# Optimization experiments

Hardware: AMD Instinct MI355X
Metric: run time of the kernel (lower is better)

## Reference

```python
import jax, jax.numpy as jnp
import numpy as np

STATE_DIM = 256
ACT_LEN = 16
LATENT = 256
ENC = 512
SLOPE = 0.01  # torch.nn.LeakyReLU() default


def _leaky(x):
    return jnp.where(x >= 0, x, SLOPE * x)


def setup_inputs() -> dict:
    key = jax.random.key(0)
    ks = jax.random.split(key, 16)
    B, T = 64, 1024
    D = STATE_DIM + 2 * ACT_LEN
    s = lambda k, shp, fan_in: jax.random.normal(k, shp, dtype=jnp.float32) * (1.0 / np.sqrt(fan_in))
    return {
        "padded_input": jax.random.normal(ks[0], (B, T, D), dtype=jnp.float32),
        # encoder: Linear(state,enc)+leaky, Linear(enc,enc)+leaky, Linear(enc,latent)+leaky
        "enc_w1": s(ks[1], (STATE_DIM, ENC), STATE_DIM), "enc_b1": jnp.zeros((ENC,), jnp.float32),
        "enc_w2": s(ks[2], (ENC, ENC), ENC),             "enc_b2": jnp.zeros((ENC,), jnp.float32),
        "enc_w3": s(ks[3], (ENC, LATENT), ENC),          "enc_b3": jnp.zeros((LATENT,), jnp.float32),
        # latent dynamics (bias-free)
        "A_w": s(ks[4], (LATENT, LATENT), LATENT),
        "B_w": s(ks[5], (ACT_LEN, LATENT), ACT_LEN),
        # decoder: Linear(latent,enc)+leaky, Linear(enc,enc)+leaky, Linear(enc,state)
        "dec_w1": s(ks[6], (LATENT, ENC), LATENT),       "dec_b1": jnp.zeros((ENC,), jnp.float32),
        "dec_w2": s(ks[7], (ENC, ENC), ENC),             "dec_b2": jnp.zeros((ENC,), jnp.float32),
        "dec_w3": s(ks[8], (ENC, STATE_DIM), ENC),       "dec_b3": jnp.zeros((STATE_DIM,), jnp.float32),
    }


def reference(padded_input, enc_w1, enc_b1, enc_w2, enc_b2, enc_w3, enc_b3,
              A_w, B_w, dec_w1, dec_b1, dec_w2, dec_b2, dec_w3, dec_b3):
    # slice features: [state | u_t | u_t1]
    x_t = padded_input[:, :, :STATE_DIM]                       # [B,T,S]
    u_t1 = padded_input[:, :, STATE_DIM + ACT_LEN:]            # [B,T,A]

    # encoder MLP
    h = _leaky(x_t @ enc_w1 + enc_b1)
    h = _leaky(h @ enc_w2 + enc_b2)
    z_t = _leaky(h @ enc_w3 + enc_b3)                          # [B,T,L]

    # reset_probability=0, nwarmup=0: t=0 uses z_t[:,0], then pure recurrence
    # z1[t] = A z1[t-1] + B u_t1[t]
    Bu = u_t1 @ B_w                                            # [B,T,L]

    def step(prev, bu_t):
        new = prev @ A_w + bu_t                                # [B,L]
        return new, new

    _, z1 = jax.lax.scan(step, z_t[:, 0, :], jnp.swapaxes(Bu, 0, 1))
    z_t1 = jnp.swapaxes(z1, 0, 1)                              # [B,T,L]

    # decoder MLP (last layer linear)
    h = _leaky(z_t1 @ dec_w1 + dec_b1)
    h = _leaky(h @ dec_w2 + dec_b2)
    x_t1 = h @ dec_w3 + dec_b3                                 # [B,T,S]
    return x_t1
```

## Files before the change

kernel.cpp:

```cpp
#include <hip/hip_runtime.h>

constexpr int Bb  = 64;
constexpr int Tt  = 1024;
constexpr int Dd  = 288;
constexpr int Ss  = 256;
constexpr int ALa = 16;
constexpr int Ll  = 256;
constexpr int Ee  = 512;
constexpr int CC  = 8;
constexpr int NCh = 128;
constexpr int NSC = 16;
constexpr int SC  = 8;
constexpr int DEC_CHUNKS = 8;
constexpr int DEC_ROWS = (Bb*Tt)/DEC_CHUNKS;

#define LKY(v) ((v) >= 0.f ? (v) : 0.01f*(v))

using f32x4  = __attribute__((ext_vector_type(4))) float;
using short8 = __attribute__((ext_vector_type(8))) short;
typedef unsigned short ushort_t;

__device__ __forceinline__ unsigned short f2bf(float f){
  unsigned int u = __float_as_uint(f);
  u = (u + 0x7fffu + ((u >> 16) & 1u)) >> 16;
  return (unsigned short)u;
}
__device__ __forceinline__ float bf2f(unsigned short h){
  return __uint_as_float(((unsigned int)h) << 16);
}

__global__ __launch_bounds__(256) void enc_dense(
    const float* __restrict__ xin, int xstride,
    const float* __restrict__ W, const float* __restrict__ bias,
    float* __restrict__ out, int K, int N, int act)
{
  int b = blockIdx.x, col0 = blockIdx.y * 32;
  int tid = threadIdx.x;
  int tx = tid & 31, tk = tid >> 5;
  __shared__ float x[512];
  __shared__ float part[8][33];
  for (int k = tid; k < K; k += 256) x[k] = xin[(long)b*xstride + k];
  __syncthreads();
  int j = col0 + tx;
  float p0=0.f,p1=0.f,p2=0.f,p3=0.f;
  int iters = K >> 3;
  #pragma unroll 2
  for (int i = 0; i < iters; i += 4){
    int k0 = tk + 8*i;
    p0 = fmaf(x[k0     ], W[(long)(k0     )*N + j], p0);
    p1 = fmaf(x[k0 +  8], W[(long)(k0 +  8)*N + j], p1);
    p2 = fmaf(x[k0 + 16], W[(long)(k0 + 16)*N + j], p2);
    p3 = fmaf(x[k0 + 24], W[(long)(k0 + 24)*N + j], p3);
  }
  part[tk][tx] = (p0+p1)+(p2+p3);
  __syncthreads();
  if (tid < 32){
    float s = part[0][tid];
    #pragma unroll
    for (int q = 1; q < 8; ++q) s += part[q][tid];
    s += bias[col0 + tid];
    out[b*N + col0 + tid] = act ? LKY(s) : s;
  }
}

__global__ __launch_bounds__(256) void matmul_g(
    const float* __restrict__ X, const float* __restrict__ Y,
    float* __restrict__ Cf, ushort_t* __restrict__ Ch, ushort_t* __restrict__ Cl)
{
  int i = blockIdx.x;
  int tid = threadIdx.x;
  int jg = tid & 63, tk = tid >> 6;
  __shared__ float row[256];
  __shared__ float4 part[4][64];
  if (tid < 256) row[tid] = X[i*256 + tid];
  __syncthreads();
  int j4 = jg*4;
  float4 p0 = make_float4(0,0,0,0), p1 = make_float4(0,0,0,0);
  int kb = tk*64;
  #pragma unroll 4
  for (int k = kb; k < kb+64; k += 2){
    float x0 = row[k], x1 = row[k+1];
    float4 y0 = *(const float4*)&Y[(k  )*256 + j4];
    float4 y1 = *(const float4*)&Y[(k+1)*256 + j4];
    p0.x = fmaf(x0,y0.x,p0.x); p0.y = fmaf(x0,y0.y,p0.y);
    p0.z = fmaf(x0,y0.z,p0.z); p0.w = fmaf(x0,y0.w,p0.w);
    p1.x = fmaf(x1,y1.x,p1.x); p1.y = fmaf(x1,y1.y,p1.y);
    p1.z = fmaf(x1,y1.z,p1.z); p1.w = fmaf(x1,y1.w,p1.w);
  }
  p0.x+=p1.x; p0.y+=p1.y; p0.z+=p1.z; p0.w+=p1.w;
  part[tk][jg] = p0;
  __syncthreads();
  if (tid < 64){
    float4 s = part[0][tid];
    #pragma unroll
    for (int q = 1; q < 4; ++q){
      float4 v = part[q][tid];
      s.x+=v.x; s.y+=v.y; s.z+=v.z; s.w+=v.w;
    }
    int j = tid*4;
    if (Cf) *(float4*)&Cf[i*256 + j] = s;
    if (Ch){
      float vv[4] = {s.x,s.y,s.z,s.w};
      #pragma unroll
      for (int e = 0; e < 4; ++e){
        ushort_t h = f2bf(vv[e]);
        int o = ((i>>3)*256 + j + e)*8 + (i&7);
        Ch[o] = h; Cl[o] = f2bf(vv[e] - bf2f(h));
      }
    }
  }
}

__global__ __launch_bounds__(256) void prep_w(
    const float* __restrict__ W, ushort_t* __restrict__ Wh,
    ushort_t* __restrict__ Wl, int N)
{
  int o = blockIdx.x*256 + threadIdx.x;
  int j = o & 7;
  int rest = o >> 3;
  int n = rest % N;
  int t8 = rest / N;
  int k = t8*8 + j;
  float v = W[k*N + n];
  ushort_t h = f2bf(v);
  Wh[o] = h;
  Wl[o] = f2bf(v - bf2f(h));
}

__global__ __launch_bounds__(256) void prep_bw(
    const float* __restrict__ B, ushort_t* __restrict__ Bh, ushort_t* __restrict__ Bl)
{
  int o = blockIdx.x*256 + threadIdx.x;
  int j = o & 7, rest = o >> 3;
  int n = rest & 255, kq = rest >> 8;
  int k = kq*8 + j;
  float v = (k < ALa) ? B[k*256 + n] : 0.f;
  ushort_t h = f2bf(v);
  Bh[o] = h; Bl[o] = f2bf(v - bf2f(h));
}

__device__ __forceinline__ void load_afrag(
    const ushort_t* __restrict__ P, int kq, int m0, short8* dst)
{
  #pragma unroll
  for (int mt = 0; mt < 4; ++mt)
    dst[mt] = *(const short8*)&P[((long)kq*256 + m0 + mt*16)*8];
}

__global__ __launch_bounds__(256) void scan_mfma(
    const float* __restrict__ in0,
    const ushort_t* __restrict__ AtH, const ushort_t* __restrict__ AtL,
    const ushort_t* __restrict__ BtH, const ushort_t* __restrict__ BtL,
    float* __restrict__ wend, float* __restrict__ zout)
{
  int chunk = blockIdx.x;
  int tid = threadIdx.x;
  int wave = tid >> 6, lane = tid & 63;
  int quad = lane >> 4, l16 = lane & 15;
  int mwave = wave * 64;
  int m0 = mwave + l16;

  __shared__ ushort_t StH[16384];
  __shared__ ushort_t StL[16384];

  short8 Bfh[4], Bfl[4];
  #pragma unroll
  for (int mt = 0; mt < 4; ++mt){
    int off = ((quad)*256 + m0 + mt*16)*8;
    Bfh[mt] = *(const short8*)&BtH[off];
    Bfl[mt] = *(const short8*)&BtL[off];
  }

  f32x4 acc[4][4];
  #pragma unroll
  for (int mt = 0; mt < 4; ++mt)
    #pragma unroll
    for (int nt = 0; nt < 4; ++nt) acc[mt][nt] = (f32x4){0.f,0.f,0.f,0.f};

  const float* ubase[4];
  #pragma unroll
  for (int nt = 0; nt < 4; ++nt)
    ubase[nt] = in0 + (long)(nt*16 + l16)*(Tt*Dd) + (Ss + ALa) + quad*8;

  short8 Ahb[2][4], Alb[2][4];

  for (int tt = 0; tt < CC; ++tt){
    int t = chunk*CC + tt;
    float4 uq[4][2];
    #pragma unroll
    for (int nt = 0; nt < 4; ++nt){
      if (quad < 2){
        const float* up = ubase[nt] + (long)t*Dd;
        uq[nt][0] = *(const float4*)up;
        uq[nt][1] = *(const float4*)(up + 4);
      } else {
        uq[nt][0] = make_float4(0,0,0,0); uq[nt][1] = make_float4(0,0,0,0);
      }
    }

    if (tt > 0){
      load_afrag(AtH, 0*4 + quad, m0, Ahb[0]);
      load_afrag(AtL, 0*4 + quad, m0, Alb[0]);
      #pragma unroll
      for (int kt = 0; kt < 8; ++kt){
        int cur = kt & 1;
        if (kt < 7){
          load_afrag(AtH, (kt+1)*4 + quad, m0, Ahb[cur^1]);
          load_afrag(AtL, (kt+1)*4 + quad, m0, Alb[cur^1]);
        }
        short8 Sbh[4], Sbl[4];
        #pragma unroll
        for (int nt = 0; nt < 4; ++nt){
          int off = ((kt*4 + quad)*64 + nt*16 + l16)*8;
          Sbh[nt] = *(const short8*)&StH[off];
          Sbl[nt] = *(const short8*)&StL[off];
        }
        #pragma unroll
        for (int mt = 0; mt < 4; ++mt)
          #pragma unroll
          for (int nt = 0; nt < 4; ++nt){
            acc[mt][nt] = __builtin_amdgcn_mfma_f32_16x16x32_bf16(Ahb[cur][mt], Sbh[nt], acc[mt][nt], 0,0,0);
            acc[mt][nt] = __builtin_amdgcn_mfma_f32_16x16x32_bf16(Ahb[cur][mt], Sbl[nt], acc[mt][nt], 0,0,0);
            acc[mt][nt] = __builtin_amdgcn_mfma_f32_16x16x32_bf16(Alb[cur][mt], Sbh[nt], acc[mt][nt], 0,0,0);
          }
      }
    }

    short8 uh[4], ul[4];
    #pragma unroll
    for (int nt = 0; nt < 4; ++nt){
      float v[8] = {uq[nt][0].x,uq[nt][0].y,uq[nt][0].z,uq[nt][0].w,
                    uq[nt][1].x,uq[nt][1].y,uq[nt][1].z,uq[nt][1].w};
      ushort_t hs[8], ls[8];
      #pragma unroll
      for (int j = 0; j < 8; ++j){
        hs[j] = f2bf(v[j]);
        ls[j] = f2bf(v[j] - bf2f(hs[j]));
      }
      uh[nt] = *(const short8*)hs; ul[nt] = *(const short8*)ls;
    }
    #pragma unroll
    for (int mt = 0; mt < 4; ++mt)
      #pragma unroll
      for (int nt = 0; nt < 4; ++nt){
        acc[mt][nt] = __builtin_amdgcn_mfma_f32_16x16x32_bf16(Bfh[mt], uh[nt], acc[mt][nt], 0,0,0);
        acc[mt][nt] = __builtin_amdgcn_mfma_f32_16x16x32_bf16(Bfh[mt], ul[nt], acc[mt][nt], 0,0,0);
        acc[mt][nt] = __builtin_amdgcn_mfma_f32_16x16x32_bf16(Bfl[mt], uh[nt], acc[mt][nt], 0,0,0);
      }

    __syncthreads();

    #pragma unroll
    for (int mt = 0; mt < 4; ++mt){
      int mb = mwave + mt*16 + quad*4;
      #pragma unroll
      for (int nt = 0; nt < 4; ++nt){
        int n = nt*16 + l16;
        f32x4 v = acc[mt][nt];
        *(float4*)&zout[((long)n*Tt + t)*Ll + mb] = make_float4(v[0],v[1],v[2],v[3]);
        if (tt == CC-1)
          *(float4*)&wend[((long)chunk*Bb + n)*Ll + mb] = make_float4(v[0],v[1],v[2],v[3]);
        #pragma unroll
        for (int reg = 0; reg < 4; ++reg){
          int m = mb + reg;
          ushort_t h = f2bf(v[reg]);
          ushort_t l = f2bf(v[reg] - bf2f(h));
          int so = ((m>>3)*64 + n)*8 + (m&7);
          StH[so] = h; StL[so] = l;
        }
        acc[mt][nt] = (f32x4){0.f,0.f,0.f,0.f};
      }
    }
    __syncthreads();
  }
}

__device__ __forceinline__ void frag_init_state512(
    const float* __restrict__ src, ushort_t* StH, ushort_t* StL, int tid)
{
  #pragma unroll
  for (int it = 0; it < 4; ++it){
    int idx = tid + it*512;
    int m8 = idx >> 6, n = idx & 63;
    const float* p = src + (long)n*256 + m8*8;
    float4 v0 = *(const float4*)p;
    float4 v1 = *(const float4*)(p + 4);
    float vv[8] = {v0.x,v0.y,v0.z,v0.w,v1.x,v1.y,v1.z,v1.w};
    ushort_t hs[8], ls[8];
    #pragma unroll
    for (int j = 0; j < 8; ++j){
      hs[j] = f2bf(vv[j]);
      ls[j] = f2bf(vv[j] - bf2f(hs[j]));
    }
    *(uint4*)&StH[(m8*64 + n)*8] = *(const uint4*)hs;
    *(uint4*)&StL[(m8*64 + n)*8] = *(const uint4*)ls;
  }
}

__device__ __forceinline__ void p2_load_A(
    const ushort_t* __restrict__ PH, const ushort_t* __restrict__ PL,
    int wave, int lane, short8 Ah[2][8], short8 Al[2][8])
{
  int quad = lane >> 4, l16 = lane & 15;
  int m0 = wave*32 + l16;
  #pragma unroll
  for (int kt = 0; kt < 8; ++kt){
    int kq = kt*4 + quad;
    #pragma unroll
    for (int mt = 0; mt < 2; ++mt){
      Ah[mt][kt] = *(const short8*)&PH[((long)kq*256 + m0 + mt*16)*8];
      Al[mt][kt] = *(const short8*)&PL[((long)kq*256 + m0 + mt*16)*8];
    }
  }
}

__device__ __forceinline__ void ks_gemm_body(
    const ushort_t* __restrict__ PH, const ushort_t* __restrict__ PL,
    const float* __restrict__ accsrc, const float* __restrict__ bsrc,
    float* __restrict__ outp, ushort_t* StH, ushort_t* StL)
{
  int tid = threadIdx.x;
  int wave = tid >> 6, lane = tid & 63;
  int quad = lane >> 4, l16 = lane & 15;
  int mwave = wave*32;

  short8 Ah[2][8], Al[2][8];
  p2_load_A(PH, PL, wave, lane, Ah, Al);
  frag_init_state512(bsrc, StH, StL, tid);

  f32x4 acc[2][4];
  #pragma unroll
  for (int mt = 0; mt < 2; ++mt){
    int mb = mwave + mt*16 + quad*4;
    #pragma unroll
    for (int nt = 0; nt < 4; ++nt){
      int n = nt*16 + l16;
      float4 v = *(const float4*)&accsrc[(long)n*256 + mb];
      acc[mt][nt] = (f32x4){v.x, v.y, v.z, v.w};
    }
  }
  __syncthreads();

  #pragma unroll
  for (int kt = 0; kt < 8; ++kt){
    #pragma unroll
    for (int nt = 0; nt < 4; ++nt){
      int off = ((kt*4 + quad)*64 + nt*16 + l16)*8;
      short8 Sbh = *(const short8*)&StH[off];
      short8 Sbl = *(const short8*)&StL[off];
      #pragma unroll
      for (int mt = 0; mt < 2; ++mt){
        acc[mt][nt] = __builtin_amdgcn_mfma_f32_16x16x32_bf16(Ah[mt][kt], Sbh, acc[mt][nt], 0,0,0);
        acc[mt][nt] = __builtin_amdgcn_mfma_f32_16x16x32_bf16(Ah[mt][kt], Sbl, acc[mt][nt], 0,0,0);
        acc[mt][nt] = __builtin_amdgcn_mfma_f32_16x16x32_bf16(Al[mt][kt], Sbh, acc[mt][nt], 0,0,0);
      }
    }
  }

  #pragma unroll
  for (int mt = 0; mt < 2; ++mt){
    int mb = mwave + mt*16 + quad*4;
    #pragma unroll
    for (int nt = 0; nt < 4; ++nt){
      int n = nt*16 + l16;
      f32x4 v = acc[mt][nt];
      *(float4*)&outp[(long)n*256 + mb] = make_float4(v[0],v[1],v[2],v[3]);
    }
  }
}

__device__ __forceinline__ const float* ks_src(
    const float* __restrict__ in, const float* __restrict__ z0,
    const float* __restrict__ pbend, int c, int init_mode)
{
  if (!init_mode) return in + (long)c*(Bb*Ll);
  return (c == 0) ? z0 : (pbend + (long)(8*c - 1)*(Bb*Ll));
}

__global__ __launch_bounds__(512) void ks_round(
    const ushort_t* __restrict__ PH, const ushort_t* __restrict__ PL,
    const float* __restrict__ in, const float* __restrict__ z0,
    const float* __restrict__ pbend,
    float* __restrict__ out, long outStride, int d, int local_seg, int init_mode)
{
  int c = blockIdx.x;
  int tid = threadIdx.x;
  int pos = local_seg ? (c & 7) : c;
  const float* src_c = ks_src(in, z0, pbend, c, init_mode);
  float* op = out + (long)c*outStride;

  if (pos < d){
    const float4* s4p = (const float4*)src_c;
    float4* d4p = (float4*)op;
    #pragma unroll
    for (int it = 0; it < 8; ++it) d4p[tid + it*512] = s4p[tid + it*512];
    return;
  }
  const float* src_cd = ks_src(in, z0, pbend, c - d, init_mode);
  __shared__ ushort_t StH[16384], StL[16384];
  ks_gemm_body(PH, PL, src_c, src_cd, op, StH, StL);
}

__global__ __launch_bounds__(512) void replay_corr(
    const ushort_t* __restrict__ A8PH, const ushort_t* __restrict__ A8PL,
    const float* __restrict__ pb, float* __restrict__ inits)
{
  int i = blockIdx.x + 1;
  int s = blockIdx.y;
  __shared__ ushort_t StH[16384], StL[16384];
  ks_gemm_body(A8PH + (long)(i-1)*65536, A8PL + (long)(i-1)*65536,
               pb + (long)(8*s + i - 1)*(Bb*Ll),
               inits + (long)(8*s)*(Bb*Ll),
               inits + (long)(8*s + i)*(Bb*Ll), StH, StL);
}

__global__ __launch_bounds__(256) void gemm_corr(
    const float* __restrict__ inits, const ushort_t* __restrict__ AjH,
    const ushort_t* __restrict__ AjL, float* __restrict__ out)
{
  int jz = blockIdx.z;
  const ushort_t* Whp = AjH + (long)jz*65536;
  const ushort_t* Wlp = AjL + (long)jz*65536;
  __shared__ __align__(16) ushort_t Xh[4*128*8], Xl[4*128*8];
  __shared__ __align__(16) ushort_t Wh[4*128*8], Wl[4*128*8];

  int tid  = threadIdx.x;
  int wave = tid >> 6, lane = tid & 63;
  int wm = wave & 1, wn = wave >> 1;
  int quad = lane >> 4, l16 = lane & 15;
  int row0 = blockIdx.y * 128;
  int col0 = blockIdx.x * 128;

  f32x4 acc[4][4];
  #pragma unroll
  for (int mt = 0; mt < 4; ++mt)
    #pragma unroll
    for (int nt = 0; nt < 4; ++nt) acc[mt][nt] = (f32x4){0.f,0.f,0.f,0.f};

  for (int kt = 0; kt < 8; ++kt){
    #pragma unroll
    for (int it = 0; it < 2; ++it){
      int idx = tid + it*256;
      int q = idx >> 7, m = idx & 127;
      const float* xp = &inits[(long)(row0 + m)*256 + kt*32 + q*8];
      float4 v0 = *(const float4*)xp;
      float4 v1 = *(const float4*)(xp + 4);
      float vv[8] = {v0.x,v0.y,v0.z,v0.w,v1.x,v1.y,v1.z,v1.w};
      ushort_t hs[8], ls[8];
      #pragma unroll
      for (int j = 0; j < 8; ++j){
        hs[j] = f2bf(vv[j]);
        ls[j] = f2bf(vv[j] - bf2f(hs[j]));
      }
      *(uint4*)&Xh[(q*128 + m)*8] = *(const uint4*)hs;
      *(uint4*)&Xl[(q*128 + m)*8] = *(const uint4*)ls;
      int n = idx & 127;
      long src = (long)(kt*4 + q)*256 + col0 + n;
      ((uint4*)Wh)[q*128 + n] = ((const uint4*)Whp)[src];
      ((uint4*)Wl)[q*128 + n] = ((const uint4*)Wlp)[src];
    }
    __syncthreads();
    short8 ah[4], al[4], bh[4], bl[4];
    #pragma unroll
    for (int mt = 0; mt < 4; ++mt){
      int off = (quad*128 + wm*64 + mt*16 + l16)*8;
      ah[mt] = *(const short8*)&Xh[off];
      al[mt] = *(const short8*)&Xl[off];
    }
    #pragma unroll
    for (int nt = 0; nt < 4; ++nt){
      int off = (quad*128 + wn*64 + nt*16 + l16)*8;
      bh[nt] = *(const short8*)&Wh[off];
      bl[nt] = *(const short8*)&Wl[off];
    }
    #pragma unroll
    for (int mt = 0; mt < 4; ++mt)
      #pragma unroll
      for (int nt = 0; nt < 4; ++nt){
        acc[mt][nt] = __builtin_amdgcn_mfma_f32_16x16x32_bf16(ah[mt], bh[nt], acc[mt][nt], 0,0,0);
        acc[mt][nt] = __builtin_amdgcn_mfma_f32_16x16x32_bf16(ah[mt], bl[nt], acc[mt][nt], 0,0,0);
        acc[mt][nt] = __builtin_amdgcn_mfma_f32_16x16x32_bf16(al[mt], bh[nt], acc[mt][nt], 0,0,0);
      }
    __syncthreads();
  }

  #pragma unroll
  for (int mt = 0; mt < 4; ++mt){
    #pragma unroll
    for (int nt = 0; nt < 4; ++nt){
      int col = col0 + wn*64 + nt*16 + l16;
      #pragma unroll
      for (int reg = 0; reg < 4; ++reg){
        int row = row0 + wm*64 + mt*16 + quad*4 + reg;
        int b = row & 63, c = row >> 6;
        int t = c*CC + jz;
        long addr = ((long)b*Tt + t)*Ll + col;
        out[addr] += acc[mt][nt][reg];
      }
    }
  }
}

template<int BM, int BN, bool INS, bool OUTS>
__global__ __launch_bounds__(256) void gemm_mfma(
    const float* __restrict__ X,
    const ushort_t* __restrict__ Xhp, const ushort_t* __restrict__ Xlp,
    const ushort_t* __restrict__ Whp, const ushort_t* __restrict__ Wlp,
    const float* __restrict__ bias, float* __restrict__ Y,
    ushort_t* __restrict__ Yh, ushort_t* __restrict__ Yl,
    int Mrows, int K, int N, int act)
{
  constexpr int BMh = BM/2, BNh = BN/2;
  constexpr int MT = BM/32, NT = BN/32;
  __shared__ __align__(16) ushort_t Xh[4*BM*8], Xl[4*BM*8];
  __shared__ __align__(16) ushort_t Wh[4*BN*8], Wl[4*BN*8];

  int tid  = threadIdx.x;
  int wave = tid >> 6, lane = tid & 63;
  int wm = wave & 1, wn = wave >> 1;
  int quad = lane >> 4, l16 = lane & 15;
  long row0 = (long)blockIdx.y * BM;
  int col0 = blockIdx.x * BN;

  f32x4 acc[MT][NT];
  #pragma unroll
  for (int mt = 0; mt < MT; ++mt)
    #pragma unroll
    for (int nt = 0; nt < NT; ++nt) acc[mt][nt] = (f32x4){0.f,0.f,0.f,0.f};

  for (int kt = 0; kt < K; kt += 32){
    int ktile = kt >> 5;
    if constexpr (INS){
      #pragma unroll
      for (int it = 0; it < (BM*4)/256; ++it){
        int idx = tid + it*256;
        int q = idx / BM, m = idx % BM;
        long src = (long)(ktile*4 + q)*Mrows + row0 + m;
        ((uint4*)Xh)[q*BM + m] = ((const uint4*)Xhp)[src];
        ((uint4*)Xl)[q*BM + m] = ((const uint4*)Xlp)[src];
      }
    } else {
      #pragma unroll
      for (int it = 0; it < (BM*4)/256; ++it){
        int idx = tid + it*256;
        int q = idx / BM, m = idx % BM;
        const float* xp = &X[(row0 + m)*(long)K + kt + q*8];
        float4 v0 = *(const float4*)xp;
        float4 v1 = *(const float4*)(xp + 4);
        float vv[8] = {v0.x,v0.y,v0.z,v0.w,v1.x,v1.y,v1.z,v1.w};
        ushort_t hs[8], ls[8];
        #pragma unroll
        for (int j = 0; j < 8; ++j){
          hs[j] = f2bf(vv[j]);
          ls[j] = f2bf(vv[j] - bf2f(hs[j]));
        }
        *(uint4*)&Xh[(q*BM + m)*8] = *(const uint4*)hs;
        *(uint4*)&Xl[(q*BM + m)*8] = *(const uint4*)ls;
      }
    }
    #pragma unroll
    for (int it = 0; it < (BN*4)/256; ++it){
      int idx = tid + it*256;
      int q = idx / BN, n = idx % BN;
      long src = (long)(ktile*4 + q)*N + col0 + n;
      ((uint4*)Wh)[q*BN + n] = ((const uint4*)Whp)[src];
      ((uint4*)Wl)[q*BN + n] = ((const uint4*)Wlp)[src];
    }
    __syncthreads();

    short8 ah[MT], al[MT], bh[NT], bl[NT];
    #pragma unroll
    for (int mt = 0; mt < MT; ++mt){
      int off = (quad*BM + wm*BMh + mt*16 + l16)*8;
      ah[mt] = *(const short8*)&Xh[off];
      al[mt] = *(const short8*)&Xl[off];
    }
    #pragma unroll
    for (int nt = 0; nt < NT; ++nt){
      int off = (quad*BN + wn*BNh + nt*16 + l16)*8;
      bh[nt] = *(const short8*)&Wh[off];
      bl[nt] = *(const short8*)&Wl[off];
    }
    #pragma unroll
    for (int mt = 0; mt < MT; ++mt)
      #pragma unroll
      for (int nt = 0; nt < NT; ++nt){
        acc[mt][nt] = __builtin_amdgcn_mfma_f32_16x16x32_bf16(ah[mt], bh[nt], acc[mt][nt], 0, 0, 0);
        acc[mt][nt] = __builtin_amdgcn_mfma_f32_16x16x32_bf16(ah[mt], bl[nt], acc[mt][nt], 0, 0, 0);
        acc[mt][nt] = __builtin_amdgcn_mfma_f32_16x16x32_bf16(al[mt], bh[nt], acc[mt][nt], 0, 0, 0);
      }
    __syncthreads();
  }

  #pragma unroll
  for (int mt = 0; mt < MT; ++mt){
    long rowb = row0 + wm*BMh + mt*16 + quad*4;
    #pragma unroll
    for (int nt = 0; nt < NT; ++nt){
      int col = col0 + wn*BNh + nt*16 + l16;
      float bs = bias[col];
      #pragma unroll
      for (int reg = 0; reg < 4; ++reg){
        float y = acc[mt][nt][reg] + bs;
        if (act) y = LKY(y);
        long row = rowb + reg;
        if constexpr (OUTS){
          ushort_t h = f2bf(y);
          ushort_t l = f2bf(y - bf2f(h));
          long off = ((long)(col >> 3)*Mrows + row)*8 + (col & 7);
          Yh[off] = h; Yl[off] = l;
        } else {
          Y[row*(long)N + col] = y;
        }
      }
    }
  }
}

extern "C" void kernel_launch(void* const* d_in, const int* in_sizes, int n_in,
                              void* d_out, int out_size, void* d_ws, size_t ws_size,
                              hipStream_t stream) {
  const float* in0    = (const float*)d_in[0];
  const float* enc_w1 = (const float*)d_in[1];
  const float* enc_b1 = (const float*)d_in[2];
  const float* enc_w2 = (const float*)d_in[3];
  const float* enc_b2 = (const float*)d_in[4];
  const float* enc_w3 = (const float*)d_in[5];
  const float* enc_b3 = (const float*)d_in[6];
  const float* A_w    = (const float*)d_in[7];
  const float* B_w    = (const float*)d_in[8];
  const float* dec_w1 = (const float*)d_in[9];
  const float* dec_b1 = (const float*)d_in[10];
  const float* dec_w2 = (const float*)d_in[11];
  const float* dec_b2 = (const float*)d_in[12];
  const float* dec_w3 = (const float*)d_in[13];
  const float* dec_b3 = (const float*)d_in[14];
  float* out = (float*)d_out;

  float* ws    = (float*)d_ws;
  float* h1enc = ws;
  float* h2enc = ws + 32768;
  float* s2    = ws + 65536;
  float* s3    = ws + 131072;
  float* s4    = ws + 196608;
  float* s8    = ws + 262144;
  float* s16   = ws + 327680;
  float* s32   = ws + 393216;
  float* s64   = ws + 458752;
  ushort_t* Whp_d = (ushort_t*)(ws + 524288);
  ushort_t* Wlp_d = (ushort_t*)(ws + 786432);
  float* Rf    = ws + 1048576;
  ushort_t* AjH = (ushort_t*)Rf;
  ushort_t* AjL = (ushort_t*)(Rf + 262144);
  ushort_t* BtH = (ushort_t*)(Rf + 524288);
  ushort_t* BtL = BtH + 8192;
  float* wend  = Rf + 532480;
  float* inits = Rf + 2629632;
  float* g0    = Rf + 4726784;
  ushort_t* A64H = (ushort_t*)(Rf + 4988928);
  ushort_t* A64L = (ushort_t*)(Rf + 5021696);
  float* pb0   = Rf + 5054464;
  ushort_t* A8PH = (ushort_t*)(Rf + 7151616);
  ushort_t* A8PL = (ushort_t*)(Rf + 7380992);
  ushort_t* A64PH = (ushort_t*)(Rf + 7610368);
  ushort_t* A64PL = (ushort_t*)(Rf + 7708672);
  float* f24   = Rf + 7806976;
  float* f128  = Rf + 7872512;
  float* f256  = Rf + 7938048;
  float* g1    = Rf + 8003584;
  ushort_t* h1h = (ushort_t*)Rf;
  ushort_t* h1l = (ushort_t*)(Rf + 2097152);
  ushort_t* h2h = (ushort_t*)(Rf + 4194304);
  ushort_t* h2l = (ushort_t*)(Rf + 6291456);
  ushort_t* A8H = AjH + 7*65536;
  ushort_t* A8L = AjL + 7*65536;

  enc_dense<<<dim3(64,16), 256, 0, stream>>>(in0, Tt*Dd, enc_w1, enc_b1, h1enc, 256, 512, 1);
  enc_dense<<<dim3(64,16), 256, 0, stream>>>(h1enc, 512, enc_w2, enc_b2, h2enc, 512, 512, 1);
  enc_dense<<<dim3(64, 8), 256, 0, stream>>>(h2enc, 512, enc_w3, enc_b3, inits, 512, 256, 1);

  prep_w<<<256, 256, 0, stream>>>(A_w, AjH, AjL, 256);
  prep_bw<<<32, 256, 0, stream>>>(B_w, BtH, BtL);
  matmul_g<<<256, 256, 0, stream>>>(A_w, A_w, s2, AjH+1*65536, AjL+1*65536);
  matmul_g<<<256, 256, 0, stream>>>(s2, A_w, s3, AjH+2*65536, AjL+2*65536);
  matmul_g<<<256, 256, 0, stream>>>(s2, s2, s4, AjH+3*65536, AjL+3*65536);
  matmul_g<<<256, 256, 0, stream>>>(s4, A_w, nullptr, AjH+4*65536, AjL+4*65536);
  matmul_g<<<256, 256, 0, stream>>>(s4, s2, nullptr, AjH+5*65536, AjL+5*65536);
  matmul_g<<<256, 256, 0, stream>>>(s4, s3, nullptr, AjH+6*65536, AjL+6*65536);
  matmul_g<<<256, 256, 0, stream>>>(s4, s4, s8, A8H, A8L);
  prep_w<<<256, 256, 0, stream>>>(s8, A8PH, A8PL, 256);
  matmul_g<<<256, 256, 0, stream>>>(s8, s8, s16, A8PH+1*65536, A8PL+1*65536);
  matmul_g<<<256, 256, 0, stream>>>(s16, s8, f24, A8PH+2*65536, A8PL+2*65536);
  matmul_g<<<256, 256, 0, stream>>>(s16, s16, s32, A8PH+3*65536, A8PL+3*65536);
  matmul_g<<<256, 256, 0, stream>>>(s32, s8, nullptr, A8PH+4*65536, A8PL+4*65536);
  matmul_g<<<256, 256, 0, stream>>>(s32, s16, nullptr, A8PH+5*65536, A8PL+5*65536);
  matmul_g<<<256, 256, 0, stream>>>(s32, f24, nullptr, A8PH+6*65536, A8PL+6*65536);
  matmul_g<<<256, 256, 0, stream>>>(s32, s32, s64, A64H, A64L);
  matmul_g<<<256, 256, 0, stream>>>(s64, s64, f128, A64PH+0*65536, A64PL+0*65536);
  matmul_g<<<256, 256, 0, stream>>>(f128, f128, f256, A64PH+1*65536, A64PL+1*65536);
  matmul_g<<<256, 256, 0, stream>>>(f256, f256, nullptr, A64PH+2*65536, A64PL+2*65536);

  prep_w<<<512,  256, 0, stream>>>(dec_w1, Whp_d,          Wlp_d,          512);
  prep_w<<<1024, 256, 0, stream>>>(dec_w2, Whp_d + 131072, Wlp_d + 131072, 512);
  prep_w<<<512,  256, 0, stream>>>(dec_w3, Whp_d + 393216, Wlp_d + 393216, 256);

  scan_mfma<<<NCh, 256, 0, stream>>>(in0, AjH, AjL, BtH, BtL, wend, out);

  ks_round<<<128, 512, 0, stream>>>(A8H, A8L, wend, nullptr, nullptr, pb0, Bb*Ll, 1, 1, 0);
  ks_round<<<128, 512, 0, stream>>>(A8PH+1*65536, A8PL+1*65536, pb0, nullptr, nullptr, wend, Bb*Ll, 2, 1, 0);
  ks_round<<<128, 512, 0, stream>>>(A8PH+3*65536, A8PL+3*65536, wend, nullptr, nullptr, pb0, Bb*Ll, 4, 1, 0);
  ks_round<<<16, 512, 0, stream>>>(A64H, A64L, nullptr, inits, pb0, g1, Bb*Ll, 1, 0, 1);
  ks_round<<<16, 512, 0, stream>>>(A64PH+0*65536, A64PL+0*65536, g1, nullptr, nullptr, g0, Bb*Ll, 2, 0, 0);
  ks_round<<<16, 512, 0, stream>>>(A64PH+1*65536, A64PL+1*65536, g0, nullptr, nullptr, g1, Bb*Ll, 4, 0, 0);
  ks_round<<<16, 512, 0, stream>>>(A64PH+2*65536, A64PL+2*65536, g1, nullptr, nullptr, inits, (long)SC*Bb*Ll, 8, 0, 0);
  replay_corr<<<dim3(7, 16), 512, 0, stream>>>(A8PH, A8PL, pb0, inits);

  gemm_corr<<<dim3(2, 64, 8), 256, 0, stream>>>(inits, AjH, AjL, out);

  for (int rc = 0; rc < DEC_CHUNKS; ++rc){
    const float* zc = out + (long)rc*DEC_ROWS*Ll;
    float* oc       = out + (long)rc*DEC_ROWS*Ll;
    gemm_mfma<64,128,false,true><<<dim3(Ee/128, DEC_ROWS/64), 256, 0, stream>>>(
        zc, nullptr, nullptr, Whp_d, Wlp_d, dec_b1, nullptr, h1h, h1l, DEC_ROWS, Ll, Ee, 1);
    gemm_mfma<64,128,true,true><<<dim3(Ee/128, DEC_ROWS/64), 256, 0, stream>>>(
        nullptr, h1h, h1l, Whp_d + 131072, Wlp_d + 131072, dec_b2, nullptr, h2h, h2l, DEC_ROWS, Ee, Ee, 1);
    gemm_mfma<64,128,true,false><<<dim3(Ss/128, DEC_ROWS/64), 256, 0, stream>>>(
        nullptr, h2h, h2l, Whp_d + 393216, Wlp_d + 393216, dec_b3, oc, nullptr, nullptr, DEC_ROWS, Ee, Ss, 0);
  }
}
```

Baseline: 984.5 us.

## Fuse encoder layers, batch power matmuls, split scan over batch halves

Merges the three encoder dense kernels into one per-batch kernel, and batches the independent matrix-power products into multi-job launches so fewer kernels run back to back. The prep kernels are also merged, and the separate A8 prep conversion is dropped by having replay_corr read A8 directly. The scan kernel gains a second grid dimension that splits the 64 batch columns into two halves, doubling the block count for the serial recurrence at the cost of loading the A fragments twice. The aim is to cut launch overhead and raise occupancy in the latency-bound prologue and scan.

```diff
diff --git a/kernel.cpp b/kernel.cpp
--- a/kernel.cpp
+++ b/kernel.cpp
@@ -29,50 +29,56 @@
   return __uint_as_float(((unsigned int)h) << 16);
 }
 
-__global__ __launch_bounds__(256) void enc_dense(
-    const float* __restrict__ xin, int xstride,
-    const float* __restrict__ W, const float* __restrict__ bias,
-    float* __restrict__ out, int K, int N, int act)
-{
-  int b = blockIdx.x, col0 = blockIdx.y * 32;
-  int tid = threadIdx.x;
-  int tx = tid & 31, tk = tid >> 5;
-  __shared__ float x[512];
-  __shared__ float part[8][33];
-  for (int k = tid; k < K; k += 256) x[k] = xin[(long)b*xstride + k];
+__global__ __launch_bounds__(256) void enc_fused(
+    const float* __restrict__ in0,
+    const float* __restrict__ w1, const float* __restrict__ b1,
+    const float* __restrict__ w2, const float* __restrict__ b2,
+    const float* __restrict__ w3, const float* __restrict__ b3,
+    float* __restrict__ z0)
+{
+  int b = blockIdx.x, tid = threadIdx.x;
+  __shared__ float xb[512], h1[512];
+  xb[tid] = (tid < 256) ? in0[(long)b*(Tt*Dd) + tid] : 0.f;
   __syncthreads();
-  int j = col0 + tx;
-  float p0=0.f,p1=0.f,p2=0.f,p3=0.f;
-  int iters = K >> 3;
-  #pragma unroll 2
-  for (int i = 0; i < iters; i += 4){
-    int k0 = tk + 8*i;
-    p0 = fmaf(x[k0     ], W[(long)(k0     )*N + j], p0);
-    p1 = fmaf(x[k0 +  8], W[(long)(k0 +  8)*N + j], p1);
-    p2 = fmaf(x[k0 + 16], W[(long)(k0 + 16)*N + j], p2);
-    p3 = fmaf(x[k0 + 24], W[(long)(k0 + 24)*N + j], p3);
-  }
-  part[tk][tx] = (p0+p1)+(p2+p3);
+  float a0 = b1[tid], a1 = b1[tid+256];
+  #pragma unroll 4
+  for (int k = 0; k < 256; ++k){
+    float xv = xb[k];
+    a0 = fmaf(xv, w1[k*512 + tid      ], a0);
+    a1 = fmaf(xv, w1[k*512 + tid + 256], a1);
+  }
   __syncthreads();
-  if (tid < 32){
-    float s = part[0][tid];
-    #pragma unroll
-    for (int q = 1; q < 8; ++q) s += part[q][tid];
-    s += bias[col0 + tid];
-    out[b*N + col0 + tid] = act ? LKY(s) : s;
-  }
-}
-
-__global__ __launch_bounds__(256) void matmul_g(
-    const float* __restrict__ X, const float* __restrict__ Y,
-    float* __restrict__ Cf, ushort_t* __restrict__ Ch, ushort_t* __restrict__ Cl)
-{
+  h1[tid] = LKY(a0); h1[tid+256] = LKY(a1);
+  __syncthreads();
+  float c0 = b2[tid], c1 = b2[tid+256];
+  #pragma unroll 4
+  for (int k = 0; k < 512; ++k){
+    float hv = h1[k];
+    c0 = fmaf(hv, w2[k*512 + tid      ], c0);
+    c1 = fmaf(hv, w2[k*512 + tid + 256], c1);
+  }
+  __syncthreads();
+  xb[tid] = LKY(c0); xb[tid+256] = LKY(c1);
+  __syncthreads();
+  float d0 = b3[tid];
+  #pragma unroll 4
+  for (int k = 0; k < 512; ++k)
+    d0 = fmaf(xb[k], w3[k*256 + tid], d0);
+  z0[b*256 + tid] = LKY(d0);
+}
+
+struct MMJob { const float* X; const float* Y; float* Cf; ushort_t* Ch; ushort_t* Cl; };
+struct MMJobs { MMJob j[4]; };
+
+__global__ __launch_bounds__(256) void matmul_gb(MMJobs jobs)
+{
+  MMJob jb = jobs.j[blockIdx.y];
   int i = blockIdx.x;
   int tid = threadIdx.x;
   int jg = tid & 63, tk = tid >> 6;
   __shared__ float row[256];
   __shared__ float4 part[4][64];
-  if (tid < 256) row[tid] = X[i*256 + tid];
+  if (tid < 256) row[tid] = jb.X[i*256 + tid];
   __syncthreads();
   int j4 = jg*4;
   float4 p0 = make_float4(0,0,0,0), p1 = make_float4(0,0,0,0);
@@ -80,8 +86,8 @@
   #pragma unroll 4
   for (int k = kb; k < kb+64; k += 2){
     float x0 = row[k], x1 = row[k+1];
-    float4 y0 = *(const float4*)&Y[(k  )*256 + j4];
-    float4 y1 = *(const float4*)&Y[(k+1)*256 + j4];
+    float4 y0 = *(const float4*)&jb.Y[(k  )*256 + j4];
+    float4 y1 = *(const float4*)&jb.Y[(k+1)*256 + j4];
     p0.x = fmaf(x0,y0.x,p0.x); p0.y = fmaf(x0,y0.y,p0.y);
     p0.z = fmaf(x0,y0.z,p0.z); p0.w = fmaf(x0,y0.w,p0.w);
     p1.x = fmaf(x1,y1.x,p1.x); p1.y = fmaf(x1,y1.y,p1.y);
@@ -98,45 +104,61 @@
       s.x+=v.x; s.y+=v.y; s.z+=v.z; s.w+=v.w;
     }
     int j = tid*4;
-    if (Cf) *(float4*)&Cf[i*256 + j] = s;
-    if (Ch){
+    if (jb.Cf) *(float4*)&jb.Cf[i*256 + j] = s;
+    if (jb.Ch){
       float vv[4] = {s.x,s.y,s.z,s.w};
       #pragma unroll
       for (int e = 0; e < 4; ++e){
         ushort_t h = f2bf(vv[e]);
         int o = ((i>>3)*256 + j + e)*8 + (i&7);
-        Ch[o] = h; Cl[o] = f2bf(vv[e] - bf2f(h));
-      }
-    }
-  }
-}
-
-__global__ __launch_bounds__(256) void prep_w(
-    const float* __restrict__ W, ushort_t* __restrict__ Wh,
-    ushort_t* __restrict__ Wl, int N)
+        jb.Ch[o] = h; jb.Cl[o] = f2bf(vv[e] - bf2f(h));
+      }
+    }
+  }
+}
+
+__global__ __launch_bounds__(256) void prep_a1bw(
+    const float* __restrict__ A, const float* __restrict__ B,
+    ushort_t* __restrict__ AH, ushort_t* __restrict__ AL,
+    ushort_t* __restrict__ Bh, ushort_t* __restrict__ Bl)
 {
   int o = blockIdx.x*256 + threadIdx.x;
-  int j = o & 7;
-  int rest = o >> 3;
-  int n = rest % N;
-  int t8 = rest / N;
+  if (o < 65536){
+    int j = o & 7, rest = o >> 3;
+    int n = rest & 255, t8 = rest >> 8;
+    int k = t8*8 + j;
+    float v = A[k*256 + n];
+    ushort_t h = f2bf(v);
+    AH[o] = h; AL[o] = f2bf(v - bf2f(h));
+  } else {
+    int ob = o - 65536;
+    int j = ob & 7, rest = ob >> 3;
+    int n = rest & 255, kq = rest >> 8;
+    int k = kq*8 + j;
+    float v = (k < ALa) ? B[k*256 + n] : 0.f;
+    ushort_t h = f2bf(v);
+    Bh[ob] = h; Bl[ob] = f2bf(v - bf2f(h));
+  }
+}
+
+__global__ __launch_bounds__(256) void prep_dec(
+    const float* __restrict__ w1, const float* __restrict__ w2,
+    const float* __restrict__ w3, ushort_t* __restrict__ Wh,
+    ushort_t* __restrict__ Wl)
+{
+  long o = (long)blockIdx.x*256 + threadIdx.x;
+  const float* W; ushort_t* H; ushort_t* L; int N; long oo;
+  if (o < 131072){ W = w1; H = Wh;          L = Wl;          N = 512; oo = o; }
+  else if (o < 393216){ W = w2; H = Wh + 131072; L = Wl + 131072; N = 512; oo = o - 131072; }
+  else { W = w3; H = Wh + 393216; L = Wl + 393216; N = 256; oo = o - 393216; }
+  int j = (int)(oo & 7);
+  long rest = oo >> 3;
+  int n = (int)(rest % N);
+  int t8 = (int)(rest / N);
   int k = t8*8 + j;
-  float v = W[k*N + n];
+  float v = W[(long)k*N + n];
   ushort_t h = f2bf(v);
-  Wh[o] = h;
-  Wl[o] = f2bf(v - bf2f(h));
-}
-
-__global__ __launch_bounds__(256) void prep_bw(
-    const float* __restrict__ B, ushort_t* __restrict__ Bh, ushort_t* __restrict__ Bl)
-{
-  int o = blockIdx.x*256 + threadIdx.x;
-  int j = o & 7, rest = o >> 3;
-  int n = rest & 255, kq = rest >> 8;
-  int k = kq*8 + j;
-  float v = (k < ALa) ? B[k*256 + n] : 0.f;
-  ushort_t h = f2bf(v);
-  Bh[o] = h; Bl[o] = f2bf(v - bf2f(h));
+  H[oo] = h; L[oo] = f2bf(v - bf2f(h));
 }
 
 __device__ __forceinline__ void load_afrag(
@@ -154,14 +176,15 @@
     float* __restrict__ wend, float* __restrict__ zout)
 {
   int chunk = blockIdx.x;
+  int n0 = blockIdx.y * 32;
   int tid = threadIdx.x;
   int wave = tid >> 6, lane = tid & 63;
   int quad = lane >> 4, l16 = lane & 15;
   int mwave = wave * 64;
   int m0 = mwave + l16;
 
-  __shared__ ushort_t StH[16384];
-  __shared__ ushort_t StL[16384];
+  __shared__ ushort_t StH[8192];
+  __shared__ ushort_t StL[8192];
 
   short8 Bfh[4], Bfl[4];
   #pragma unroll
@@ -171,24 +194,24 @@
     Bfl[mt] = *(const short8*)&BtL[off];
   }
 
-  f32x4 acc[4][4];
+  f32x4 acc[4][2];
   #pragma unroll
   for (int mt = 0; mt < 4; ++mt)
     #pragma unroll
-    for (int nt = 0; nt < 4; ++nt) acc[mt][nt] = (f32x4){0.f,0.f,0.f,0.f};
-
-  const float* ubase[4];
-  #pragma unroll
-  for (int nt = 0; nt < 4; ++nt)
-    ubase[nt] = in0 + (long)(nt*16 + l16)*(Tt*Dd) + (Ss + ALa) + quad*8;
+    for (int nt = 0; nt < 2; ++nt) acc[mt][nt] = (f32x4){0.f,0.f,0.f,0.f};
+
+  const float* ubase[2];
+  #pragma unroll
+  for (int nt = 0; nt < 2; ++nt)
+    ubase[nt] = in0 + (long)(n0 + nt*16 + l16)*(Tt*Dd) + (Ss + ALa) + quad*8;
 
   short8 Ahb[2][4], Alb[2][4];
 
   for (int tt = 0; tt < CC; ++tt){
     int t = chunk*CC + tt;
-    float4 uq[4][2];
-    #pragma unroll
-    for (int nt = 0; nt < 4; ++nt){
+    float4 uq[2][2];
+    #pragma unroll
+    for (int nt = 0; nt < 2; ++nt){
       if (quad < 2){
         const float* up = ubase[nt] + (long)t*Dd;
         uq[nt][0] = *(const float4*)up;
@@ -208,17 +231,17 @@
           load_afrag(AtH, (kt+1)*4 + quad, m0, Ahb[cur^1]);
           load_afrag(AtL, (kt+1)*4 + quad, m0, Alb[cur^1]);
         }
-        short8 Sbh[4], Sbl[4];
+        short8 Sbh[2], Sbl[2];
         #pragma unroll
-        for (int nt = 0; nt < 4; ++nt){
-          int off = ((kt*4 + quad)*64 + nt*16 + l16)*8;
+        for (int nt = 0; nt < 2; ++nt){
+          int off = ((kt*4 + quad)*32 + nt*16 + l16)*8;
           Sbh[nt] = *(const short8*)&StH[off];
           Sbl[nt] = *(const short8*)&StL[off];
         }
         #pragma unroll
         for (int mt = 0; mt < 4; ++mt)
           #pragma unroll
-          for (int nt = 0; nt < 4; ++nt){
+          for (int nt = 0; nt < 2; ++nt){
             acc[mt][nt] = __builtin_amdgcn_mfma_f32_16x16x32_bf16(Ahb[cur][mt], Sbh[nt], acc[mt][nt], 0,0,0);
             acc[mt][nt] = __builtin_amdgcn_mfma_f32_16x16x32_bf16(Ahb[cur][mt], Sbl[nt], acc[mt][nt], 0,0,0);
             acc[mt][nt] = __builtin_amdgcn_mfma_f32_16x16x32_bf16(Alb[cur][mt], Sbh[nt], acc[mt][nt], 0,0,0);
@@ -226,9 +249,9 @@
       }
     }
 
-    short8 uh[4], ul[4];
-    #pragma unroll
-    for (int nt = 0; nt < 4; ++nt){
+    short8 uh[2], ul[2];
+    #pragma unroll
+    for (int nt = 0; nt < 2; ++nt){
       float v[8] = {uq[nt][0].x,uq[nt][0].y,uq[nt][0].z,uq[nt][0].w,
                     uq[nt][1].x,uq[nt][1].y,uq[nt][1].z,uq[nt][1].w};
       ushort_t hs[8], ls[8];
@@ -242,7 +265,7 @@
     #pragma unroll
     for (int mt = 0; mt < 4; ++mt)
       #pragma unroll
-      for (int nt = 0; nt < 4; ++nt){
+      for (int nt = 0; nt < 2; ++nt){
         acc[mt][nt] = __builtin_amdgcn_mfma_f32_16x16x32_bf16(Bfh[mt], uh[nt], acc[mt][nt], 0,0,0);
         acc[mt][nt] = __builtin_amdgcn_mfma_f32_16x16x32_bf16(Bfh[mt], ul[nt], acc[mt][nt], 0,0,0);
         acc[mt][nt] = __builtin_amdgcn_mfma_f32_16x16x32_bf16(Bfl[mt], uh[nt], acc[mt][nt], 0,0,0);
@@ -254,18 +277,19 @@
     for (int mt = 0; mt < 4; ++mt){
       int mb = mwave + mt*16 + quad*4;
       #pragma unroll
-      for (int nt = 0; nt < 4; ++nt){
+      for (int nt = 0; nt < 2; ++nt){
         int n = nt*16 + l16;
+        int gn = n0 + n;
         f32x4 v = acc[mt][nt];
-        *(float4*)&zout[((long)n*Tt + t)*Ll + mb] = make_float4(v[0],v[1],v[2],v[3]);
+        *(float4*)&zout[((long)gn*Tt + t)*Ll + mb] = make_float4(v[0],v[1],v[2],v[3]);
         if (tt == CC-1)
-          *(float4*)&wend[((long)chunk*Bb + n)*Ll + mb] = make_float4(v[0],v[1],v[2],v[3]);
+          *(float4*)&wend[((long)chunk*Bb + gn)*Ll + mb] = make_float4(v[0],v[1],v[2],v[3]);
         #pragma unroll
         for (int reg = 0; reg < 4; ++reg){
           int m = mb + reg;
           ushort_t h = f2bf(v[reg]);
           ushort_t l = f2bf(v[reg] - bf2f(h));
-          int so = ((m>>3)*64 + n)*8 + (m&7);
+          int so = ((m>>3)*32 + n)*8 + (m&7);
           StH[so] = h; StL[so] = l;
         }
         acc[mt][nt] = (f32x4){0.f,0.f,0.f,0.f};
@@ -402,13 +426,16 @@
 }
 
 __global__ __launch_bounds__(512) void replay_corr(
+    const ushort_t* __restrict__ A8H, const ushort_t* __restrict__ A8L,
     const ushort_t* __restrict__ A8PH, const ushort_t* __restrict__ A8PL,
     const float* __restrict__ pb, float* __restrict__ inits)
 {
   int i = blockIdx.x + 1;
   int s = blockIdx.y;
+  const ushort_t* PH = (i == 1) ? A8H : (A8PH + (long)(i-1)*65536);
+  const ushort_t* PL = (i == 1) ? A8L : (A8PL + (long)(i-1)*65536);
   __shared__ ushort_t StH[16384], StL[16384];
-  ks_gemm_body(A8PH + (long)(i-1)*65536, A8PL + (long)(i-1)*65536,
+  ks_gemm_body(PH, PL,
                pb + (long)(8*s + i - 1)*(Bb*Ll),
                inits + (long)(8*s)*(Bb*Ll),
                inits + (long)(8*s + i)*(Bb*Ll), StH, StL);
@@ -638,8 +665,6 @@
   float* out = (float*)d_out;
 
   float* ws    = (float*)d_ws;
-  float* h1enc = ws;
-  float* h2enc = ws + 32768;
   float* s2    = ws + 65536;
   float* s3    = ws + 131072;
   float* s4    = ws + 196608;
@@ -675,36 +700,53 @@
   ushort_t* A8H = AjH + 7*65536;
   ushort_t* A8L = AjL + 7*65536;
 
-  enc_dense<<<dim3(64,16), 256, 0, stream>>>(in0, Tt*Dd, enc_w1, enc_b1, h1enc, 256, 512, 1);
-  enc_dense<<<dim3(64,16), 256, 0, stream>>>(h1enc, 512, enc_w2, enc_b2, h2enc, 512, 512, 1);
-  enc_dense<<<dim3(64, 8), 256, 0, stream>>>(h2enc, 512, enc_w3, enc_b3, inits, 512, 256, 1);
-
-  prep_w<<<256, 256, 0, stream>>>(A_w, AjH, AjL, 256);
-  prep_bw<<<32, 256, 0, stream>>>(B_w, BtH, BtL);
-  matmul_g<<<256, 256, 0, stream>>>(A_w, A_w, s2, AjH+1*65536, AjL+1*65536);
-  matmul_g<<<256, 256, 0, stream>>>(s2, A_w, s3, AjH+2*65536, AjL+2*65536);
-  matmul_g<<<256, 256, 0, stream>>>(s2, s2, s4, AjH+3*65536, AjL+3*65536);
-  matmul_g<<<256, 256, 0, stream>>>(s4, A_w, nullptr, AjH+4*65536, AjL+4*65536);
-  matmul_g<<<256, 256, 0, stream>>>(s4, s2, nullptr, AjH+5*65536, AjL+5*65536);
-  matmul_g<<<256, 256, 0, stream>>>(s4, s3, nullptr, AjH+6*65536, AjL+6*65536);
-  matmul_g<<<256, 256, 0, stream>>>(s4, s4, s8, A8H, A8L);
-  prep_w<<<256, 256, 0, stream>>>(s8, A8PH, A8PL, 256);
-  matmul_g<<<256, 256, 0, stream>>>(s8, s8, s16, A8PH+1*65536, A8PL+1*65536);
-  matmul_g<<<256, 256, 0, stream>>>(s16, s8, f24, A8PH+2*65536, A8PL+2*65536);
-  matmul_g<<<256, 256, 0, stream>>>(s16, s16, s32, A8PH+3*65536, A8PL+3*65536);
-  matmul_g<<<256, 256, 0, stream>>>(s32, s8, nullptr, A8PH+4*65536, A8PL+4*65536);
-  matmul_g<<<256, 256, 0, stream>>>(s32, s16, nullptr, A8PH+5*65536, A8PL+5*65536);
-  matmul_g<<<256, 256, 0, stream>>>(s32, f24, nullptr, A8PH+6*65536, A8PL+6*65536);
-  matmul_g<<<256, 256, 0, stream>>>(s32, s32, s64, A64H, A64L);
-  matmul_g<<<256, 256, 0, stream>>>(s64, s64, f128, A64PH+0*65536, A64PL+0*65536);
-  matmul_g<<<256, 256, 0, stream>>>(f128, f128, f256, A64PH+1*65536, A64PL+1*65536);
-  matmul_g<<<256, 256, 0, stream>>>(f256, f256, nullptr, A64PH+2*65536, A64PL+2*65536);
-
-  prep_w<<<512,  256, 0, stream>>>(dec_w1, Whp_d,          Wlp_d,          512);
-  prep_w<<<1024, 256, 0, stream>>>(dec_w2, Whp_d + 131072, Wlp_d + 131072, 512);
-  prep_w<<<512,  256, 0, stream>>>(dec_w3, Whp_d + 393216, Wlp_d + 393216, 256);
-
-  scan_mfma<<<NCh, 256, 0, stream>>>(in0, AjH, AjL, BtH, BtL, wend, out);
+  enc_fused<<<64, 256, 0, stream>>>(in0, enc_w1, enc_b1, enc_w2, enc_b2,
+                                    enc_w3, enc_b3, inits);
+
+  prep_a1bw<<<288, 256, 0, stream>>>(A_w, B_w, AjH, AjL, BtH, BtL);
+
+  auto mj = [](const float* X, const float* Y, float* Cf, ushort_t* Ch, ushort_t* Cl){
+    MMJob r; r.X = X; r.Y = Y; r.Cf = Cf; r.Ch = Ch; r.Cl = Cl; return r;
+  };
+  { MMJobs J = {};
+    J.j[0] = mj(A_w, A_w, s2, AjH+1*65536, AjL+1*65536);
+    matmul_gb<<<dim3(256,1), 256, 0, stream>>>(J); }
+  { MMJobs J = {};
+    J.j[0] = mj(s2, A_w, s3, AjH+2*65536, AjL+2*65536);
+    J.j[1] = mj(s2, s2,  s4, AjH+3*65536, AjL+3*65536);
+    matmul_gb<<<dim3(256,2), 256, 0, stream>>>(J); }
+  { MMJobs J = {};
+    J.j[0] = mj(s4, A_w, nullptr, AjH+4*65536, AjL+4*65536);
+    J.j[1] = mj(s4, s2,  nullptr, AjH+5*65536, AjL+5*65536);
+    J.j[2] = mj(s4, s3,  nullptr, AjH+6*65536, AjL+6*65536);
+    J.j[3] = mj(s4, s4,  s8, A8H, A8L);
+    matmul_gb<<<dim3(256,4), 256, 0, stream>>>(J); }
+  { MMJobs J = {};
+    J.j[0] = mj(s8, s8, s16, A8PH+1*65536, A8PL+1*65536);
+    matmul_gb<<<dim3(256,1), 256, 0, stream>>>(J); }
+  { MMJobs J = {};
+    J.j[0] = mj(s16, s8,  f24, A8PH+2*65536, A8PL+2*65536);
+    J.j[1] = mj(s16, s16, s32, A8PH+3*65536, A8PL+3*65536);
+    matmul_gb<<<dim3(256,2), 256, 0, stream>>>(J); }
+  { MMJobs J = {};
+    J.j[0] = mj(s32, s8,  nullptr, A8PH+4*65536, A8PL+4*65536);
+    J.j[1] = mj(s32, s16, nullptr, A8PH+5*65536, A8PL+5*65536);
+    J.j[2] = mj(s32, f24, nullptr, A8PH+6*65536, A8PL+6*65536);
+    J.j[3] = mj(s32, s32, s64, A64H, A64L);
+    matmul_gb<<<dim3(256,4), 256, 0, stream>>>(J); }
+  { MMJobs J = {};
+    J.j[0] = mj(s64, s64, f128, A64PH+0*65536, A64PL+0*65536);
+    matmul_gb<<<dim3(256,1), 256, 0, stream>>>(J); }
+  { MMJobs J = {};
+    J.j[0] = mj(f128, f128, f256, A64PH+1*65536, A64PL+1*65536);
+    matmul_gb<<<dim3(256,1), 256, 0, stream>>>(J); }
+  { MMJobs J = {};
+    J.j[0] = mj(f256, f256, nullptr, A64PH+2*65536, A64PL+2*65536);
+    matmul_gb<<<dim3(256,1), 256, 0, stream>>>(J); }
+
+  prep_dec<<<2048, 256, 0, stream>>>(dec_w1, dec_w2, dec_w3, Whp_d, Wlp_d);
+
+  scan_mfma<<<dim3(NCh, 2), 256, 0, stream>>>(in0, AjH, AjL, BtH, BtL, wend, out);
 
   ks_round<<<128, 512, 0, stream>>>(A8H, A8L, wend, nullptr, nullptr, pb0, Bb*Ll, 1, 1, 0);
   ks_round<<<128, 512, 0, stream>>>(A8PH+1*65536, A8PL+1*65536, pb0, nullptr, nullptr, wend, Bb*Ll, 2, 1, 0);
@@ -713,7 +755,7 @@
   ks_round<<<16, 512, 0, stream>>>(A64PH+0*65536, A64PL+0*65536, g1, nullptr, nullptr, g0, Bb*Ll, 2, 0, 0);
   ks_round<<<16, 512, 0, stream>>>(A64PH+1*65536, A64PL+1*65536, g0, nullptr, nullptr, g1, Bb*Ll, 4, 0, 0);
   ks_round<<<16, 512, 0, stream>>>(A64PH+2*65536, A64PL+2*65536, g1, nullptr, nullptr, inits, (long)SC*Bb*Ll, 8, 0, 0);
-  replay_corr<<<dim3(7, 16), 512, 0, stream>>>(A8PH, A8PL, pb0, inits);
+  replay_corr<<<dim3(7, 16), 512, 0, stream>>>(A8H, A8L, A8PH, A8PL, pb0, inits);
 
   gemm_corr<<<dim3(2, 64, 8), 256, 0, stream>>>(inits, AjH, AjL, out);
 
```

Result: slower. 1.021 ms (+3.7%).
